# Optimization experiments

Measured on AMD Instinct MI355X. Metric: run time of the kernel, lower is better.

The kernel has to match this reference:

```python
import jax, jax.numpy as jnp
import numpy as np


def _normalize(x):
    # F.normalize(x, dim=-1): x / max(||x||_2, eps)
    n = jnp.linalg.norm(x, axis=-1, keepdims=True)
    return x / jnp.maximum(n, 1e-12)


def _clip_loss(i_sh, t_sh, scale, y):
    # Faithful, vectorized version of CLIP.forward (y: [B,1] int labels).
    i_n = _normalize(i_sh)
    t_n = _normalize(t_sh)
    logit_i2t = (i_n @ t_n.T) * scale            # [B,B]
    logit_t2i = t_n @ i_n.T                      # NOTE: no scale, as in source
    bs = i_sh.shape[0]
    yv = y.reshape(-1)                           # [B]
    # y.expand(bs,bs).T with y [bs,1] -> base[k,j] = y[j]
    base = jnp.broadcast_to(yv[None, :], (bs, bs)).astype(i_sh.dtype)
    flipped = jnp.where(base == 0, 1.0, 0.0)     # the inner loop flips 0<->nonzero
    label = jnp.where(yv[:, None] == 0, flipped, base)
    q = jax.nn.softmax(label / label.sum(axis=-1, keepdims=True), axis=-1)
    lq = jnp.log(q)
    lp1 = jax.nn.log_softmax(logit_i2t, axis=-1)
    lp2 = jax.nn.log_softmax(logit_t2i, axis=-1)
    # F.kl_div(input=log_pred, target, 'batchmean') = sum(target*(log(target)-input))/bs
    kl_p1_q = jnp.sum(q * (lq - lp1)) / bs
    kl_q_p1 = jnp.sum(jnp.exp(lp1) * (lp1 - lq)) / bs
    kl_p2_q = jnp.sum(q * (lq - lp2)) / bs
    kl_q_p2 = jnp.sum(jnp.exp(lp2) * (lp2 - lq)) / bs
    return (kl_p1_q + kl_q_p1 + kl_p2_q + kl_q_p2) / 4.0


def _forward(i, t, y, l1_w, l1_b, l2_w, l2_b, l3_w, l3_b, tl1_w, tl1_b, tl2_w, tl2_b,
             isp_w, isp_b, ish_w, ish_b, tsh_w, tsh_b, tsp_w, tsp_b,
             c1_w, c1_b, c2_w, c2_b, c3_w, c3_b, c4_w, c4_b, scale1, scale2):
    # ImgEncoder MLP head (penet backbone replaced by pooled 2048-d features;
    # dropout = identity, eval semantics)
    fi = jax.nn.relu(i @ l1_w.T + l1_b)
    fi = jax.nn.relu(fi @ l2_w.T + l2_b)
    fi = fi @ l3_w.T + l3_b                       # [B,128]
    # TabEncoder
    ft = jax.nn.relu(t @ tl1_w.T + tl1_b)
    ft = ft @ tl2_w.T + tl2_b                     # [B,128]
    loss1 = _clip_loss(fi, ft, jnp.exp(scale1), y)
    # SS heads
    i_sp = fi @ isp_w.T + isp_b
    i_sh = fi @ ish_w.T + ish_b
    t_sh = ft @ tsh_w.T + tsh_b
    t_sp = ft @ tsp_w.T + tsp_b
    # Separate: mean of Frobenius norms of BxB cross-Grams
    loss_sp = (jnp.linalg.norm(t_sp @ t_sh.T) + jnp.linalg.norm(i_sp @ i_sh.T)) / 2.0
    loss_sh = _clip_loss(i_sh, t_sh, jnp.exp(scale2), y)
    loss = (loss_sp + loss_sh + loss1) / 3.0
    i_sp_out = i_sp @ c1_w.T + c1_b
    i_sh_out = i_sh @ c2_w.T + c2_b
    t_sh_out = t_sh @ c3_w.T + c3_b
    t_sp_out = t_sp @ c4_w.T + c4_b
    return (loss, i_sp_out, i_sh_out, t_sp_out, t_sh_out)


def setup_inputs() -> dict:
    key = jax.random.key(0)
    ks = jax.random.split(key, 20)
    B = 4096

    def lin(k, out_d, in_d):  # kaiming-normal fan_out, relu
        return jax.random.normal(k, (out_d, in_d), jnp.float32) * np.sqrt(2.0 / out_d)

    log_scale = jnp.asarray(np.log(1.0 / 0.07), jnp.float32)
    return {
        'i': jax.random.normal(ks[0], (B, 2048), jnp.float32),
        't': jax.random.normal(ks[1], (B, 49), jnp.float32),
        'y': jax.random.randint(ks[2], (B, 1), 0, 2, jnp.int64 if jax.config.read('jax_enable_x64') else jnp.int32),
        'l1_w': lin(ks[3], 512, 2048), 'l1_b': jnp.zeros((512,), jnp.float32),
        'l2_w': lin(ks[4], 256, 512), 'l2_b': jnp.zeros((256,), jnp.float32),
        'l3_w': lin(ks[5], 128, 256), 'l3_b': jnp.zeros((128,), jnp.float32),
        'tl1_w': lin(ks[6], 128, 49), 'tl1_b': jnp.zeros((128,), jnp.float32),
        'tl2_w': lin(ks[7], 128, 128), 'tl2_b': jnp.zeros((128,), jnp.float32),
        'isp_w': lin(ks[8], 128, 128), 'isp_b': jnp.zeros((128,), jnp.float32),
        'ish_w': lin(ks[9], 128, 128), 'ish_b': jnp.zeros((128,), jnp.float32),
        'tsh_w': lin(ks[10], 128, 128), 'tsh_b': jnp.zeros((128,), jnp.float32),
        'tsp_w': lin(ks[11], 128, 128), 'tsp_b': jnp.zeros((128,), jnp.float32),
        'c1_w': lin(ks[12], 1, 128), 'c1_b': jnp.zeros((1,), jnp.float32),
        'c2_w': lin(ks[13], 1, 128), 'c2_b': jnp.zeros((1,), jnp.float32),
        'c3_w': lin(ks[14], 1, 128), 'c3_b': jnp.zeros((1,), jnp.float32),
        'c4_w': lin(ks[15], 1, 128), 'c4_b': jnp.zeros((1,), jnp.float32),
        'scale1': log_scale, 'scale2': log_scale,
    }


def reference(i, t, y, l1_w, l1_b, l2_w, l2_b, l3_w, l3_b, tl1_w, tl1_b, tl2_w, tl2_b,
              isp_w, isp_b, ish_w, ish_b, tsh_w, tsh_b, tsp_w, tsp_b,
              c1_w, c1_b, c2_w, c2_b, c3_w, c3_b, c4_w, c4_b, scale1, scale2):
    return _forward(i, t, y, l1_w, l1_b, l2_w, l2_b, l3_w, l3_b, tl1_w, tl1_b, tl2_w, tl2_b,
                    isp_w, isp_b, ish_w, ish_b, tsh_w, tsh_b, tsp_w, tsp_b,
                    c1_w, c1_b, c2_w, c2_b, c3_w, c3_b, c4_w, c4_b, scale1, scale2)
```

## Files before the change

### kernel.cpp

```cpp
#include <hip/hip_runtime.h>
#include <math.h>

#define BSZ 4096

typedef __attribute__((ext_vector_type(8))) short bf16x8;
typedef __attribute__((ext_vector_type(4))) float f32x4;

#define ST_ROW 0
#define ST_COL 786432
#define ST_T   1572864
#define ST_FLOATS 1589248

__device__ __forceinline__ unsigned short f2b(float f) {
    unsigned u = __float_as_uint(f);
    u = u + 0x7fffu + ((u >> 16) & 1u);
    return (unsigned short)(u >> 16);
}
__device__ __forceinline__ float b2f(unsigned short s) {
    return __uint_as_float(((unsigned)s) << 16);
}

__global__ void cast_all(const float* __restrict__ i_in,
                         const float* __restrict__ l1, const float* __restrict__ l2,
                         const float* __restrict__ l3, const float* __restrict__ tl2,
                         const float* __restrict__ isp, const float* __restrict__ ish,
                         const float* __restrict__ tsh, const float* __restrict__ tsp,
                         unsigned short* __restrict__ o) {
    int i = (blockIdx.x * 256 + threadIdx.x) * 4;
    if (i >= 9682944) return;
    const float* src; int off;
    if (i < 8388608)      { src = i_in; off = 0; }
    else if (i < 9437184) { src = l1;  off = 8388608; }
    else if (i < 9568256) { src = l2;  off = 9437184; }
    else if (i < 9601024) { src = l3;  off = 9568256; }
    else if (i < 9617408) { src = tl2; off = 9601024; }
    else if (i < 9633792) { src = isp; off = 9617408; }
    else if (i < 9650176) { src = ish; off = 9633792; }
    else if (i < 9666560) { src = tsh; off = 9650176; }
    else                  { src = tsp; off = 9666560; }
    float4 v = *(const float4*)(src + (i - off));
    ushort4 r;
    r.x = f2b(v.x); r.y = f2b(v.y); r.z = f2b(v.z); r.w = f2b(v.w);
    *(ushort4*)(o + i) = r;
}

__global__ void gemm_small(const float* __restrict__ A, const float* __restrict__ W,
                           const float* __restrict__ bias, unsigned short* __restrict__ C,
                           int M, int N, int K, int relu) {
    __shared__ float As[16][65];
    __shared__ float Ws[16][65];
    const int tx = threadIdx.x, ty = threadIdx.y;
    const int tid = ty * 16 + tx;
    const int m0 = blockIdx.y * 64, n0 = blockIdx.x * 64;
    float acc[4][4] = {};
    const int lrow = tid >> 2;
    const int lkb = (tid & 3) * 4;
    for (int k0 = 0; k0 < K; k0 += 16) {
#pragma unroll
        for (int u = 0; u < 4; ++u) {
            int k = k0 + lkb + u;
            As[lkb + u][lrow] = (k < K) ? A[(size_t)(m0 + lrow) * K + k] : 0.0f;
            Ws[lkb + u][lrow] = (k < K) ? W[(size_t)(n0 + lrow) * K + k] : 0.0f;
        }
        __syncthreads();
#pragma unroll
        for (int kk = 0; kk < 16; ++kk) {
            float av[4], bv[4];
#pragma unroll
            for (int i = 0; i < 4; ++i) av[i] = As[kk][ty * 4 + i];
#pragma unroll
            for (int j = 0; j < 4; ++j) bv[j] = Ws[kk][tx * 4 + j];
#pragma unroll
            for (int i = 0; i < 4; ++i)
#pragma unroll
                for (int j = 0; j < 4; ++j) acc[i][j] += av[i] * bv[j];
        }
        __syncthreads();
    }
#pragma unroll
    for (int i = 0; i < 4; ++i)
#pragma unroll
        for (int j = 0; j < 4; ++j) {
            int n = n0 + tx * 4 + j;
            float v = acc[i][j] + bias[n];
            if (relu) v = fmaxf(v, 0.0f);
            C[(size_t)(m0 + ty * 4 + i) * N + n] = f2b(v);
        }
}

__device__ __forceinline__ void mfma_loop(const unsigned short* __restrict__ A,
                                          const unsigned short* __restrict__ W,
                                          int K, int m0, int n0,
                                          short* As, short* Bs, f32x4 (&acc)[4][4]) {
    const int tid = threadIdx.x;
    const int w = tid >> 6, lane = tid & 63, quad = lane >> 4, l15 = lane & 15;
    const int rw = (w >> 1) * 64, cw = (w & 1) * 64;
    for (int k0 = 0; k0 < K; k0 += 64) {
#pragma unroll
        for (int r = 0; r < 4; ++r) {
            int idx = r * 256 + tid;
            int row = idx >> 3, cbp = idx & 7;
            int col = ((cbp ^ (row & 7)) << 3);
            *(bf16x8*)&As[row * 64 + cbp * 8] = *(const bf16x8*)&A[(size_t)(m0 + row) * K + k0 + col];
            *(bf16x8*)&Bs[row * 64 + cbp * 8] = *(const bf16x8*)&W[(size_t)(n0 + row) * K + k0 + col];
        }
        __syncthreads();
#pragma unroll
        for (int kb = 0; kb < 2; ++kb) {
            bf16x8 af[4], bfr[4];
            int cb = kb * 4 + quad;
#pragma unroll
            for (int i = 0; i < 4; ++i) {
                int row = rw + i * 16 + l15;
                af[i] = *(const bf16x8*)&As[row * 64 + ((cb ^ (row & 7)) << 3)];
            }
#pragma unroll
            for (int j = 0; j < 4; ++j) {
                int row = cw + j * 16 + l15;
                bfr[j] = *(const bf16x8*)&Bs[row * 64 + ((cb ^ (row & 7)) << 3)];
            }
#pragma unroll
            for (int i = 0; i < 4; ++i)
#pragma unroll
                for (int j = 0; j < 4; ++j)
                    acc[i][j] = __builtin_amdgcn_mfma_f32_16x16x32_bf16(af[i], bfr[j], acc[i][j], 0, 0, 0);
        }
        __syncthreads();
    }
}

__global__ __launch_bounds__(256) void mfma_gemm(const unsigned short* __restrict__ A,
                                                 const unsigned short* __restrict__ W,
                                                 const float* __restrict__ bias,
                                                 unsigned short* __restrict__ Cb,
                                                 int N, int K, int relu) {
    __shared__ alignas(16) short As[128 * 64];
    __shared__ alignas(16) short Bs[128 * 64];
    const int tid = threadIdx.x;
    const int w = tid >> 6, lane = tid & 63, quad = lane >> 4, l15 = lane & 15;
    const int rw = (w >> 1) * 64, cw = (w & 1) * 64;
    const int m0 = blockIdx.y * 128, n0 = blockIdx.x * 128;
    f32x4 acc[4][4];
#pragma unroll
    for (int i = 0; i < 4; ++i)
#pragma unroll
        for (int j = 0; j < 4; ++j) acc[i][j] = (f32x4){0.f, 0.f, 0.f, 0.f};
    mfma_loop(A, W, K, m0, n0, As, Bs, acc);
#pragma unroll
    for (int j = 0; j < 4; ++j) {
        int n = n0 + cw + j * 16 + l15;
        float bv = bias[n];
#pragma unroll
        for (int i = 0; i < 4; ++i)
#pragma unroll
            for (int r = 0; r < 4; ++r) {
                int m = m0 + rw + i * 16 + quad * 4 + r;
                float v = acc[i][j][r] + bv;
                if (relu) v = fmaxf(v, 0.f);
                Cb[(size_t)m * N + n] = f2b(v);
            }
    }
}

__global__ __launch_bounds__(256) void gemm34n(const unsigned short* __restrict__ FI2B,
                                               const unsigned short* __restrict__ FT1B,
                                               const unsigned short* __restrict__ WB,
                                               const float* __restrict__ l3_b,
                                               const float* __restrict__ tl2_b,
                                               unsigned short* __restrict__ FIB,
                                               unsigned short* __restrict__ FTB,
                                               unsigned short* __restrict__ FINB,
                                               unsigned short* __restrict__ FTNB) {
    __shared__ alignas(16) short As[128 * 64];
    __shared__ alignas(16) short Bs[128 * 64];
    __shared__ float rowss[128];
    const int tid = threadIdx.x;
    if (tid < 128) rowss[tid] = 0.f;
    const int z = blockIdx.z;
    const unsigned short* A = z ? FT1B : FI2B;
    const unsigned short* W = z ? (WB + 1212416) : (WB + 1179648);
    const float* bias = z ? tl2_b : l3_b;
    unsigned short* Cb = z ? FTB : FIB;
    unsigned short* CN = z ? FTNB : FINB;
    const int K = z ? 128 : 256;
    const int w = tid >> 6, lane = tid & 63, quad = lane >> 4, l15 = lane & 15;
    const int rw = (w >> 1) * 64, cw = (w & 1) * 64;
    const int m0 = blockIdx.y * 128;
    f32x4 acc[4][4];
#pragma unroll
    for (int i = 0; i < 4; ++i)
#pragma unroll
        for (int j = 0; j < 4; ++j) acc[i][j] = (f32x4){0.f, 0.f, 0.f, 0.f};
    mfma_loop(A, W, K, m0, 0, As, Bs, acc);
    float bv[4];
#pragma unroll
    for (int j = 0; j < 4; ++j) bv[j] = bias[cw + j * 16 + l15];
#pragma unroll
    for (int i = 0; i < 4; ++i)
#pragma unroll
        for (int r = 0; r < 4; ++r) {
            float ssp = 0.f;
#pragma unroll
            for (int j = 0; j < 4; ++j) {
                float v = acc[i][j][r] + bv[j];
                ssp += v * v;
            }
#pragma unroll
            for (int m = 1; m < 16; m <<= 1) ssp += __shfl_xor(ssp, m);
            if (l15 == 0) atomicAdd(&rowss[rw + i * 16 + quad * 4 + r], ssp);
        }
    __syncthreads();
#pragma unroll
    for (int i = 0; i < 4; ++i)
#pragma unroll
        for (int r = 0; r < 4; ++r) {
            int lrow = rw + i * 16 + quad * 4 + r;
            float inv = 1.f / fmaxf(sqrtf(rowss[lrow]), 1e-12f);
#pragma unroll
            for (int j = 0; j < 4; ++j) {
                int n = cw + j * 16 + l15;
                float v = acc[i][j][r] + bv[j];
                Cb[(size_t)(m0 + lrow) * 128 + n] = f2b(v);
                CN[(size_t)(m0 + lrow) * 128 + n] = f2b(v * inv);
            }
        }
}

__global__ __launch_bounds__(256) void heads4f(const unsigned short* __restrict__ FIB,
                                               const unsigned short* __restrict__ FTB,
                                               const unsigned short* __restrict__ WB,
                                               const float* __restrict__ bisp, const float* __restrict__ bish,
                                               const float* __restrict__ btsh, const float* __restrict__ btsp,
                                               const float* __restrict__ c1w, const float* __restrict__ c2w,
                                               const float* __restrict__ c3w, const float* __restrict__ c4w,
                                               const float* __restrict__ c1b, const float* __restrict__ c2b,
                                               const float* __restrict__ c3b, const float* __restrict__ c4b,
                                               float* __restrict__ ISP, float* __restrict__ ISH,
                                               float* __restrict__ TSH, float* __restrict__ TSP,
                                               unsigned short* __restrict__ ISHN,
                                               unsigned short* __restrict__ TSHN,
                                               float* __restrict__ out) {
    __shared__ alignas(16) short As[128 * 64];
    __shared__ alignas(16) short Bs[128 * 64];
    __shared__ float rowss[128];
    __shared__ float rowdot[128];
    const int tid = threadIdx.x;
    if (tid < 128) { rowss[tid] = 0.f; rowdot[tid] = 0.f; }
    const int z = blockIdx.z;
    const unsigned short* A = (z < 2) ? FIB : FTB;
    const unsigned short* W = WB + (z == 0 ? 1228800 : z == 1 ? 1245184 : z == 2 ? 1261568 : 1277952);
    const float* bias = z == 0 ? bisp : z == 1 ? bish : z == 2 ? btsh : btsp;
    const float* hw = z == 0 ? c1w : z == 1 ? c2w : z == 2 ? c3w : c4w;
    const float* hb = z == 0 ? c1b : z == 1 ? c2b : z == 2 ? c3b : c4b;
    float* Cf = z == 0 ? ISP : z == 1 ? ISH : z == 2 ? TSH : TSP;
    unsigned short* CN = z == 1 ? ISHN : z == 2 ? TSHN : nullptr;
    const int outoff = z == 0 ? 0 : z == 1 ? 1 : z == 2 ? 3 : 2;
    const int do_norm = (z == 1 || z == 2);
    const int w = tid >> 6, lane = tid & 63, quad = lane >> 4, l15 = lane & 15;
    const int rw = (w >> 1) * 64, cw = (w & 1) * 64;
    const int m0 = blockIdx.y * 128;
    f32x4 acc[4][4];
#pragma unroll
    for (int i = 0; i < 4; ++i)
#pragma unroll
        for (int j = 0; j < 4; ++j) acc[i][j] = (f32x4){0.f, 0.f, 0.f, 0.f};
    mfma_loop(A, W, 128, m0, 0, As, Bs, acc);
    float bv[4], wv[4];
#pragma unroll
    for (int j = 0; j < 4; ++j) {
        int n = cw + j * 16 + l15;
        bv[j] = bias[n];
        wv[j] = hw[n];
    }
#pragma unroll
    for (int i = 0; i < 4; ++i)
#pragma unroll
        for (int r = 0; r < 4; ++r) {
            float ssp = 0.f, dp = 0.f;
#pragma unroll
            for (int j = 0; j < 4; ++j) {
                float v = acc[i][j][r] + bv[j];
                ssp += v * v;
                dp += v * wv[j];
            }
#pragma unroll
            for (int m = 1; m < 16; m <<= 1) {
                ssp += __shfl_xor(ssp, m);
                dp += __shfl_xor(dp, m);
            }
            if (l15 == 0) {
                int lrow = rw + i * 16 + quad * 4 + r;
                atomicAdd(&rowdot[lrow], dp);
                if (do_norm) atomicAdd(&rowss[lrow], ssp);
            }
        }
    __syncthreads();
#pragma unroll
    for (int i = 0; i < 4; ++i)
#pragma unroll
        for (int r = 0; r < 4; ++r) {
            int lrow = rw + i * 16 + quad * 4 + r;
            float inv = do_norm ? (1.f / fmaxf(sqrtf(rowss[lrow]), 1e-12f)) : 0.f;
#pragma unroll
            for (int j = 0; j < 4; ++j) {
                int n = cw + j * 16 + l15;
                float v = acc[i][j][r] + bv[j];
                Cf[(size_t)(m0 + lrow) * 128 + n] = v;
                if (do_norm) CN[(size_t)(m0 + lrow) * 128 + n] = f2b(v * inv);
            }
        }
    if (tid < 128) out[1 + (size_t)outoff * BSZ + m0 + tid] = rowdot[tid] + hb[0];
}

__global__ __launch_bounds__(256) void clip_mfma(const unsigned short* __restrict__ In1,
                                                 const unsigned short* __restrict__ Tn1,
                                                 const unsigned short* __restrict__ In2,
                                                 const unsigned short* __restrict__ Tn2,
                                                 const int* __restrict__ y,
                                                 const float* __restrict__ scale_log1,
                                                 const float* __restrict__ scale_log2,
                                                 float* __restrict__ st1, float* __restrict__ st2) {
    __shared__ alignas(16) short As[128 * 64];
    __shared__ alignas(16) short Bs[128 * 64];
    const int z = blockIdx.z;
    const unsigned short* In = z ? In2 : In1;
    const unsigned short* Tn = z ? Tn2 : Tn1;
    const float* scale_log = z ? scale_log2 : scale_log1;
    float* st = z ? st2 : st1;
    const int tid = threadIdx.x;
    const int w = tid >> 6, lane = tid & 63, quad = lane >> 4, l15 = lane & 15;
    const int bx = blockIdx.x, by = blockIdx.y;
    const int r0 = by * 128, c0 = bx * 128;
    const int rw = (w >> 1) * 64, cw = (w & 1) * 64;
    f32x4 acc[4][4];
#pragma unroll
    for (int i = 0; i < 4; ++i)
#pragma unroll
        for (int j = 0; j < 4; ++j) acc[i][j] = (f32x4){0.f, 0.f, 0.f, 0.f};
    mfma_loop(In, Tn, 128, r0, c0, As, Bs, acc);

    const float s = expf(scale_log[0]);
    int yrow[4][4]; float mrow[4][4];
    int ycol[4];    float mcol[4];
#pragma unroll
    for (int i = 0; i < 4; ++i)
#pragma unroll
        for (int r = 0; r < 4; ++r) {
            int yy = y[r0 + rw + i * 16 + quad * 4 + r];
            yrow[i][r] = yy; mrow[i][r] = (yy == 0) ? 1.f : 0.f;
        }
#pragma unroll
    for (int j = 0; j < 4; ++j) {
        int yy = y[c0 + cw + j * 16 + l15];
        ycol[j] = yy; mcol[j] = (yy == 0) ? 1.f : 0.f;
    }
    float rZ[4][4] = {}, rF[4][4] = {}, rW[4][4] = {};
    float cZ[4] = {}, cE[4] = {}, cW[4] = {};
    float aAll = 0.f, aC0 = 0.f, aR0 = 0.f, aRC = 0.f;
#pragma unroll
    for (int i = 0; i < 4; ++i)
#pragma unroll
        for (int r = 0; r < 4; ++r) {
            float mr = mrow[i][r];
            int yr = yrow[i][r];
#pragma unroll
            for (int j = 0; j < 4; ++j) {
                float S = acc[i][j][r];
                float L = s * S;
                float e1 = __expf(L);
                float e2 = __expf(S);
                float msk = (yr == ycol[j]) ? 1.f : 0.f;
                rZ[i][r] += e1; rF[i][r] += e1 * L; rW[i][r] += e1 * msk;
                cZ[j] += e2;    cE[j] += e2 * S;    cW[j] += e2 * msk;
                float tmp = S * mcol[j];
                aAll += S; aC0 += tmp; aR0 += S * mr; aRC += tmp * mr;
            }
        }
    const int p_row = bx * 2 + (cw >> 6);
#pragma unroll
    for (int i = 0; i < 4; ++i)
#pragma unroll
        for (int r = 0; r < 4; ++r) {
#pragma unroll
            for (int m = 1; m < 16; m <<= 1) {
                rZ[i][r] += __shfl_xor(rZ[i][r], m);
                rF[i][r] += __shfl_xor(rF[i][r], m);
                rW[i][r] += __shfl_xor(rW[i][r], m);
            }
            if (l15 == (i * 4 + r)) {
                int grow = r0 + rw + i * 16 + quad * 4 + r;
                int base = ST_ROW + p_row * 4096 + grow;
                st[base]          = rZ[i][r];
                st[base + 262144] = rF[i][r];
                st[base + 524288] = rW[i][r];
            }
        }
    const int p_col = by * 2 + (rw >> 6);
#pragma unroll
    for (int j = 0; j < 4; ++j) {
        cZ[j] += __shfl_xor(cZ[j], 16); cZ[j] += __shfl_xor(cZ[j], 32);
        cE[j] += __shfl_xor(cE[j], 16); cE[j] += __shfl_xor(cE[j], 32);
        cW[j] += __shfl_xor(cW[j], 16); cW[j] += __shfl_xor(cW[j], 32);
        if (quad == 0) {
            int gcol = c0 + cw + j * 16 + l15;
            int base = ST_COL + p_col * 4096 + gcol;
            st[base]          = cZ[j];
            st[base + 262144] = cE[j];
            st[base + 524288] = cW[j];
        }
    }
#pragma unroll
    for (int m = 1; m < 64; m <<= 1) {
        aAll += __shfl_xor(aAll, m); aC0 += __shfl_xor(aC0, m);
        aR0 += __shfl_xor(aR0, m);   aRC += __shfl_xor(aRC, m);
    }
    if (lane == 0) {
        int wg = (by * 32 + bx) * 4 + w;
        float T00 = aRC, T01 = aR0 - aRC, T10 = aC0 - aRC, T11 = aAll - aR0 - aC0 + aRC;
        st[ST_T + wg * 4 + 0] = T00;
        st[ST_T + wg * 4 + 1] = T01;
        st[ST_T + wg * 4 + 2] = T10;
        st[ST_T + wg * 4 + 3] = T11;
    }
}

__global__ __launch_bounds__(256) void clip_finalize(const float* __restrict__ st1,
                                                     const float* __restrict__ st2,
                                                     const int* __restrict__ y,
                                                     float* __restrict__ RV,
                                                     float* __restrict__ TT) {
    __shared__ float cred[256];
    const int z = blockIdx.y;
    const float* st = z ? st2 : st1;
    const int tid = threadIdx.x;
    const int lane = tid & 63;
    const int k = blockIdx.x * 4 + (tid >> 6);
    const float Bf = (float)BSZ;

    float ccnt = 0.f;
    for (int i = tid; i < BSZ; i += 256) ccnt += (y[i] == 0) ? 1.f : 0.f;
    cred[tid] = ccnt;
    __syncthreads();
    for (int ss2 = 128; ss2 > 0; ss2 >>= 1) {
        if (tid < ss2) cred[tid] += cred[tid + ss2];
        __syncthreads();
    }
    const float n0 = cred[0];

    const int base = lane * 4096 + k;
    float Z1 = st[ST_ROW + base];
    float F1 = st[ST_ROW + 262144 + base];
    float W1 = st[ST_ROW + 524288 + base];
    float Z2 = st[ST_COL + base];
    float E2 = st[ST_COL + 262144 + base];
    float W2 = st[ST_COL + 524288 + base];
#pragma unroll
    for (int m = 1; m < 64; m <<= 1) {
        Z1 += __shfl_xor(Z1, m); F1 += __shfl_xor(F1, m); W1 += __shfl_xor(W1, m);
        Z2 += __shfl_xor(Z2, m); E2 += __shfl_xor(E2, m); W2 += __shfl_xor(W2, m);
    }
    if (lane == 0) {
        int yk = y[k];
        float n = (yk == 0) ? n0 : (Bf - n0);
        float a = 1.0f / n;
        float ea = expf(a);
        float denom = n * ea + (Bf - n);
        float q_s = ea / denom, q_d = 1.0f / denom;
        float ld = logf(denom);
        float lq_s = a - ld, lq_d = -ld;
        float Qlq = n * q_s * lq_s + (Bf - n) * q_d * lq_d;
        float term_r = Qlq + F1 / Z1 - lq_d - (lq_s - lq_d) * (W1 / Z1);
        float term_c = Qlq + E2 / Z2 - lq_d - (lq_s - lq_d) * (W2 / Z2);
        RV[(size_t)z * BSZ + k] = (term_r + term_c) / (4.0f * Bf);
    }
    if (blockIdx.x == 0) {
        __shared__ float4 tred[256];
        const float4* tp = (const float4*)&st[ST_T];
        float4 acc = {0.f, 0.f, 0.f, 0.f};
        for (int u = tid; u < 4096; u += 256) {
            float4 t4 = tp[u];
            acc.x += t4.x; acc.y += t4.y; acc.z += t4.z; acc.w += t4.w;
        }
        tred[tid] = acc;
        __syncthreads();
        for (int ss2 = 128; ss2 > 0; ss2 >>= 1) {
            if (tid < ss2) {
                tred[tid].x += tred[tid + ss2].x; tred[tid].y += tred[tid + ss2].y;
                tred[tid].z += tred[tid + ss2].z; tred[tid].w += tred[tid + ss2].w;
            }
            __syncthreads();
        }
        if (tid == 0) {
            TT[z * 4 + 0] = tred[0].x; TT[z * 4 + 1] = tred[0].y;
            TT[z * 4 + 2] = tred[0].z; TT[z * 4 + 3] = tred[0].w;
        }
    }
}

__global__ __launch_bounds__(256) void gram_splitk(const float* __restrict__ isp,
                                                   const float* __restrict__ ish,
                                                   const float* __restrict__ tsp,
                                                   const float* __restrict__ tsh,
                                                   float* __restrict__ GP) {
    __shared__ alignas(16) float As2[64][128];
    const int mat = blockIdx.y, chunk = blockIdx.x;
    const float* A = mat == 0 ? isp : mat == 1 ? ish : mat == 2 ? tsp : tsh;
    const int tid = threadIdx.x;
    const int m0 = chunk * 64;
#pragma unroll
    for (int r = 0; r < 8; ++r) {
        int idx = r * 256 + tid;
        int row = idx >> 5, c4 = (idx & 31) * 4;
        *(float4*)&As2[row][c4] = *(const float4*)&A[(size_t)(m0 + row) * 128 + c4];
    }
    __syncthreads();
    const int ty = tid >> 4, tx = tid & 15;
    float acc[8][8] = {};
    for (int k = 0; k < 64; ++k) {
        float av[8], bv[8];
        *(float4*)&av[0] = *(const float4*)&As2[k][ty * 8];
        *(float4*)&av[4] = *(const float4*)&As2[k][ty * 8 + 4];
        *(float4*)&bv[0] = *(const float4*)&As2[k][tx * 8];
        *(float4*)&bv[4] = *(const float4*)&As2[k][tx * 8 + 4];
#pragma unroll
        for (int i = 0; i < 8; ++i)
#pragma unroll
            for (int j = 0; j < 8; ++j) acc[i][j] += av[i] * bv[j];
    }
    float* Gp = GP + ((size_t)(mat * 64 + chunk) << 14);
#pragma unroll
    for (int i = 0; i < 8; ++i) {
        *(float4*)&Gp[(ty * 8 + i) * 128 + tx * 8]     = *(float4*)&acc[i][0];
        *(float4*)&Gp[(ty * 8 + i) * 128 + tx * 8 + 4] = *(float4*)&acc[i][4];
    }
}

__global__ void frob_combine(const float* __restrict__ GP, float* __restrict__ scal) {
    const int z = blockIdx.y;
    const int tid = threadIdx.x;
    int u = blockIdx.x * 256 + tid * 4;
    float4 ga = {0.f, 0.f, 0.f, 0.f};
    float4 gb = {0.f, 0.f, 0.f, 0.f};
    const size_t baseA = ((size_t)(2 * z) * 64) << 14;
    const size_t baseB = ((size_t)(2 * z + 1) * 64) << 14;
    for (int c = 0; c < 64; ++c) {
        float4 va = *(const float4*)&GP[baseA + ((size_t)c << 14) + u];
        float4 vb = *(const float4*)&GP[baseB + ((size_t)c << 14) + u];
        ga.x += va.x; ga.y += va.y; ga.z += va.z; ga.w += va.w;
        gb.x += vb.x; gb.y += vb.y; gb.z += vb.z; gb.w += vb.w;
    }
    float r = ga.x * gb.x + ga.y * gb.y + ga.z * gb.z + ga.w * gb.w;
#pragma unroll
    for (int m = 1; m < 64; m <<= 1) r += __shfl_xor(r, m);
    if (tid == 0) atomicAdd(&scal[3 + z], r);
}

__global__ void final_kernel(const float* __restrict__ RV, const float* __restrict__ scal,
                             const int* __restrict__ y,
                             const float* __restrict__ sl1, const float* __restrict__ sl2,
                             float* __restrict__ out) {
    __shared__ float red0[256], red1[256], red2[256];
    int tid = threadIdx.x;
    float s0 = 0.f, s1 = 0.f, cnt = 0.f;
    for (int u = tid; u < BSZ; u += 256) {
        s0 += RV[u]; s1 += RV[BSZ + u];
        cnt += (y[u] == 0) ? 1.f : 0.f;
    }
    red0[tid] = s0; red1[tid] = s1; red2[tid] = cnt;
    __syncthreads();
    for (int ss = 128; ss > 0; ss >>= 1) {
        if (tid < ss) {
            red0[tid] += red0[tid + ss]; red1[tid] += red1[tid + ss];
            red2[tid] += red2[tid + ss];
        }
        __syncthreads();
    }
    if (tid == 0) {
        const float Bf = (float)BSZ;
        float n0 = red2[0], n1 = Bf - n0;
        float e0 = expf(1.f / n0), e1 = expf(1.f / n1);
        float d0 = n0 * e0 + (Bf - n0), d1 = n1 * e1 + (Bf - n1);
        float qs0 = e0 / d0, qd0 = 1.f / d0, qs1 = e1 / d1, qd1 = 1.f / d1;
        float loss_z[2];
        for (int z = 0; z < 2; ++z) {
            float T00 = scal[8 + z * 4 + 0], T01 = scal[8 + z * 4 + 1];
            float T10 = scal[8 + z * 4 + 2], T11 = scal[8 + z * 4 + 3];
            float QS1 = qd0 * (T00 + T01) + (qs0 - qd0) * T00 + qd1 * (T10 + T11) + (qs1 - qd1) * T11;
            float QS2 = qd0 * (T00 + T10) + (qs0 - qd0) * T00 + qd1 * (T01 + T11) + (qs1 - qd1) * T11;
            float s = expf(z ? sl2[0] : sl1[0]);
            loss_z[z] = (z ? red1[0] : red0[0]) + (-s * QS1 - QS2) / (4.0f * Bf);
        }
        float loss_sp = 0.5f * (sqrtf(scal[4]) + sqrtf(scal[3]));
        out[0] = (loss_sp + loss_z[1] + loss_z[0]) / 3.0f;
    }
}

extern "C" void kernel_launch(void* const* d_in, const int* in_sizes, int n_in,
                              void* d_out, int out_size, void* d_ws, size_t ws_size,
                              hipStream_t stream) {
    const float* i_in  = (const float*)d_in[0];
    const float* t_in  = (const float*)d_in[1];
    const int*   y     = (const int*)d_in[2];
    const float* l1_w  = (const float*)d_in[3];
    const float* l1_b  = (const float*)d_in[4];
    const float* l2_w  = (const float*)d_in[5];
    const float* l2_b  = (const float*)d_in[6];
    const float* l3_w  = (const float*)d_in[7];
    const float* l3_b  = (const float*)d_in[8];
    const float* tl1_w = (const float*)d_in[9];
    const float* tl1_b = (const float*)d_in[10];
    const float* tl2_w = (const float*)d_in[11];
    const float* tl2_b = (const float*)d_in[12];
    const float* isp_w = (const float*)d_in[13];
    const float* isp_b = (const float*)d_in[14];
    const float* ish_w = (const float*)d_in[15];
    const float* ish_b = (const float*)d_in[16];
    const float* tsh_w = (const float*)d_in[17];
    const float* tsh_b = (const float*)d_in[18];
    const float* tsp_w = (const float*)d_in[19];
    const float* tsp_b = (const float*)d_in[20];
    const float* c1_w  = (const float*)d_in[21];
    const float* c1_b  = (const float*)d_in[22];
    const float* c2_w  = (const float*)d_in[23];
    const float* c2_b  = (const float*)d_in[24];
    const float* c3_w  = (const float*)d_in[25];
    const float* c3_b  = (const float*)d_in[26];
    const float* c4_w  = (const float*)d_in[27];
    const float* c4_b  = (const float*)d_in[28];
    const float* scale1 = (const float*)d_in[29];
    const float* scale2 = (const float*)d_in[30];

    float* ws = (float*)d_ws;
    float* SCAL = ws;
    float* RV   = ws + 64;
    float* ISP  = RV + 2 * BSZ;
    float* ISH  = ISP + (size_t)BSZ * 128;
    float* TSP  = ISH + (size_t)BSZ * 128;
    float* TSH  = TSP + (size_t)BSZ * 128;
    unsigned short* IB   = (unsigned short*)(TSH + (size_t)BSZ * 128);
    unsigned short* WB   = IB + (size_t)BSZ * 2048;
    unsigned short* FI1B = WB + 1294336;
    unsigned short* FI2B = FI1B + (size_t)BSZ * 512;
    unsigned short* FIB  = FI2B + (size_t)BSZ * 256;
    unsigned short* FT1B = FIB + (size_t)BSZ * 128;
    unsigned short* FTB  = FT1B + (size_t)BSZ * 128;
    unsigned short* FINB = FTB + (size_t)BSZ * 128;
    unsigned short* FTNB = FINB + (size_t)BSZ * 128;
    unsigned short* ISHN = FTNB + (size_t)BSZ * 128;
    unsigned short* TSHN = ISHN + (size_t)BSZ * 128;
    float* ST1 = (float*)IB;
    float* ST2 = ST1 + ST_FLOATS;
    float* GP = (float*)IB;

    float* out = (float*)d_out;

    hipMemsetAsync(d_ws, 0, 64 * sizeof(float), stream);
    cast_all<<<9456, 256, 0, stream>>>(i_in, l1_w, l2_w, l3_w, tl2_w, isp_w, ish_w, tsh_w, tsp_w, IB);
    gemm_small<<<dim3(2, 64), dim3(16, 16), 0, stream>>>(t_in, tl1_w, tl1_b, FT1B, BSZ, 128, 49, 1);

    mfma_gemm<<<dim3(4, 32), 256, 0, stream>>>(IB, WB, l1_b, FI1B, 512, 2048, 1);
    mfma_gemm<<<dim3(2, 32), 256, 0, stream>>>(FI1B, WB + 1048576, l2_b, FI2B, 256, 512, 1);
    gemm34n<<<dim3(1, 32, 2), 256, 0, stream>>>(FI2B, FT1B, WB, l3_b, tl2_b, FIB, FTB, FINB, FTNB);
    heads4f<<<dim3(1, 32, 4), 256, 0, stream>>>(FIB, FTB, WB, isp_b, ish_b, tsh_b, tsp_b,
                                                c1_w, c2_w, c3_w, c4_w, c1_b, c2_b, c3_b, c4_b,
                                                ISP, ISH, TSH, TSP, ISHN, TSHN, out);

    clip_mfma<<<dim3(32, 32, 2), 256, 0, stream>>>(FINB, FTNB, ISHN, TSHN, y, scale1, scale2, ST1, ST2);
    clip_finalize<<<dim3(1024, 2), 256, 0, stream>>>(ST1, ST2, y, RV, &SCAL[8]);

    gram_splitk<<<dim3(64, 4), 256, 0, stream>>>(ISP, ISH, TSP, TSH, GP);
    frob_combine<<<dim3(64, 2), 64, 0, stream>>>(GP, SCAL);
    final_kernel<<<1, 256, 0, stream>>>(RV, SCAL, y, scale1, scale2, out);
}
```

Baseline: 332.9 us.

## Merge small kernels, halve GEMM M-tile, and transpose clip stats layout

The cast and the small tabular GEMM now run in one launch, and the clip finalize and Gram split-K now share one launch, with GP moved to its own workspace region so the two do not overlap. The large MLP GEMMs switch to 64-row tiles, which doubles the grid for better CU occupancy at the cost of less reuse of the weight tile. The per-partition clip statistics are stored row-major (k*64+p), so the finalize reads them contiguously. Together this cuts launch overhead and idle tails, but the larger shared-memory footprint in post_kernel may reduce occupancy for the finalize blocks.

```diff
diff --git a/kernel.cpp b/kernel.cpp
--- a/kernel.cpp
+++ b/kernel.cpp
@@ -20,38 +20,40 @@
     return __uint_as_float(((unsigned)s) << 16);
 }
 
-__global__ void cast_all(const float* __restrict__ i_in,
-                         const float* __restrict__ l1, const float* __restrict__ l2,
-                         const float* __restrict__ l3, const float* __restrict__ tl2,
-                         const float* __restrict__ isp, const float* __restrict__ ish,
-                         const float* __restrict__ tsh, const float* __restrict__ tsp,
-                         unsigned short* __restrict__ o) {
-    int i = (blockIdx.x * 256 + threadIdx.x) * 4;
-    if (i >= 9682944) return;
-    const float* src; int off;
-    if (i < 8388608)      { src = i_in; off = 0; }
-    else if (i < 9437184) { src = l1;  off = 8388608; }
-    else if (i < 9568256) { src = l2;  off = 9437184; }
-    else if (i < 9601024) { src = l3;  off = 9568256; }
-    else if (i < 9617408) { src = tl2; off = 9601024; }
-    else if (i < 9633792) { src = isp; off = 9617408; }
-    else if (i < 9650176) { src = ish; off = 9633792; }
-    else if (i < 9666560) { src = tsh; off = 9650176; }
-    else                  { src = tsp; off = 9666560; }
-    float4 v = *(const float4*)(src + (i - off));
-    ushort4 r;
-    r.x = f2b(v.x); r.y = f2b(v.y); r.z = f2b(v.z); r.w = f2b(v.w);
-    *(ushort4*)(o + i) = r;
-}
-
-__global__ void gemm_small(const float* __restrict__ A, const float* __restrict__ W,
-                           const float* __restrict__ bias, unsigned short* __restrict__ C,
-                           int M, int N, int K, int relu) {
+__global__ void prep_kernel(const float* __restrict__ i_in,
+                            const float* __restrict__ l1, const float* __restrict__ l2,
+                            const float* __restrict__ l3, const float* __restrict__ tl2,
+                            const float* __restrict__ isp, const float* __restrict__ ish,
+                            const float* __restrict__ tsh, const float* __restrict__ tsp,
+                            unsigned short* __restrict__ o,
+                            const float* __restrict__ t_in, const float* __restrict__ tl1_w,
+                            const float* __restrict__ tl1_b, unsigned short* __restrict__ FT1B) {
     __shared__ float As[16][65];
     __shared__ float Ws[16][65];
-    const int tx = threadIdx.x, ty = threadIdx.y;
-    const int tid = ty * 16 + tx;
-    const int m0 = blockIdx.y * 64, n0 = blockIdx.x * 64;
+    if (blockIdx.x < 9456) {
+        int i = (blockIdx.x * 256 + threadIdx.x) * 4;
+        if (i >= 9682944) return;
+        const float* src; int off;
+        if (i < 8388608)      { src = i_in; off = 0; }
+        else if (i < 9437184) { src = l1;  off = 8388608; }
+        else if (i < 9568256) { src = l2;  off = 9437184; }
+        else if (i < 9601024) { src = l3;  off = 9568256; }
+        else if (i < 9617408) { src = tl2; off = 9601024; }
+        else if (i < 9633792) { src = isp; off = 9617408; }
+        else if (i < 9650176) { src = ish; off = 9633792; }
+        else if (i < 9666560) { src = tsh; off = 9650176; }
+        else                  { src = tsp; off = 9666560; }
+        float4 v = *(const float4*)(src + (i - off));
+        ushort4 r;
+        r.x = f2b(v.x); r.y = f2b(v.y); r.z = f2b(v.z); r.w = f2b(v.w);
+        *(ushort4*)(o + i) = r;
+        return;
+    }
+    const int b = blockIdx.x - 9456;
+    const int tid = threadIdx.x;
+    const int tx = tid & 15, ty = tid >> 4;
+    const int m0 = (b >> 1) * 64, n0 = (b & 1) * 64;
+    const int K = 49, N = 128;
     float acc[4][4] = {};
     const int lrow = tid >> 2;
     const int lkb = (tid & 3) * 4;
@@ -59,8 +61,8 @@
 #pragma unroll
         for (int u = 0; u < 4; ++u) {
             int k = k0 + lkb + u;
-            As[lkb + u][lrow] = (k < K) ? A[(size_t)(m0 + lrow) * K + k] : 0.0f;
-            Ws[lkb + u][lrow] = (k < K) ? W[(size_t)(n0 + lrow) * K + k] : 0.0f;
+            As[lkb + u][lrow] = (k < K) ? t_in[(size_t)(m0 + lrow) * K + k] : 0.0f;
+            Ws[lkb + u][lrow] = (k < K) ? tl1_w[(size_t)(n0 + lrow) * K + k] : 0.0f;
         }
         __syncthreads();
 #pragma unroll
@@ -82,9 +84,8 @@
 #pragma unroll
         for (int j = 0; j < 4; ++j) {
             int n = n0 + tx * 4 + j;
-            float v = acc[i][j] + bias[n];
-            if (relu) v = fmaxf(v, 0.0f);
-            C[(size_t)(m0 + ty * 4 + i) * N + n] = f2b(v);
+            float v = fmaxf(acc[i][j] + tl1_b[n], 0.0f);
+            FT1B[(size_t)(m0 + ty * 4 + i) * N + n] = f2b(v);
         }
 }
 
@@ -129,29 +130,66 @@
     }
 }
 
-__global__ __launch_bounds__(256) void mfma_gemm(const unsigned short* __restrict__ A,
-                                                 const unsigned short* __restrict__ W,
-                                                 const float* __restrict__ bias,
-                                                 unsigned short* __restrict__ Cb,
-                                                 int N, int K, int relu) {
-    __shared__ alignas(16) short As[128 * 64];
+__global__ __launch_bounds__(256) void mfma_gemm64(const unsigned short* __restrict__ A,
+                                                   const unsigned short* __restrict__ W,
+                                                   const float* __restrict__ bias,
+                                                   unsigned short* __restrict__ Cb,
+                                                   int N, int K, int relu) {
+    __shared__ alignas(16) short As[64 * 64];
     __shared__ alignas(16) short Bs[128 * 64];
     const int tid = threadIdx.x;
     const int w = tid >> 6, lane = tid & 63, quad = lane >> 4, l15 = lane & 15;
-    const int rw = (w >> 1) * 64, cw = (w & 1) * 64;
-    const int m0 = blockIdx.y * 128, n0 = blockIdx.x * 128;
-    f32x4 acc[4][4];
-#pragma unroll
-    for (int i = 0; i < 4; ++i)
+    const int rw = (w >> 1) * 32, cw = (w & 1) * 64;
+    const int m0 = blockIdx.y * 64, n0 = blockIdx.x * 128;
+    f32x4 acc[2][4];
+#pragma unroll
+    for (int i = 0; i < 2; ++i)
 #pragma unroll
         for (int j = 0; j < 4; ++j) acc[i][j] = (f32x4){0.f, 0.f, 0.f, 0.f};
-    mfma_loop(A, W, K, m0, n0, As, Bs, acc);
+    for (int k0 = 0; k0 < K; k0 += 64) {
+#pragma unroll
+        for (int r = 0; r < 2; ++r) {
+            int idx = r * 256 + tid;
+            int row = idx >> 3, cbp = idx & 7;
+            int col = ((cbp ^ (row & 7)) << 3);
+            *(bf16x8*)&As[row * 64 + cbp * 8] = *(const bf16x8*)&A[(size_t)(m0 + row) * K + k0 + col];
+        }
+#pragma unroll
+        for (int r = 0; r < 4; ++r) {
+            int idx = r * 256 + tid;
+            int row = idx >> 3, cbp = idx & 7;
+            int col = ((cbp ^ (row & 7)) << 3);
+            *(bf16x8*)&Bs[row * 64 + cbp * 8] = *(const bf16x8*)&W[(size_t)(n0 + row) * K + k0 + col];
+        }
+        __syncthreads();
+#pragma unroll
+        for (int kb = 0; kb < 2; ++kb) {
+            bf16x8 af[2], bfr[4];
+            int cb = kb * 4 + quad;
+#pragma unroll
+            for (int i = 0; i < 2; ++i) {
+                int row = rw + i * 16 + l15;
+                af[i] = *(const bf16x8*)&As[row * 64 + ((cb ^ (row & 7)) << 3)];
+            }
+#pragma unroll
+            for (int j = 0; j < 4; ++j) {
+                int row = cw + j * 16 + l15;
+                bfr[j] = *(const bf16x8*)&Bs[row * 64 + ((cb ^ (row & 7)) << 3)];
+            }
+#pragma unroll
+            for (int i = 0; i < 2; ++i)
+#pragma unroll
+                for (int j = 0; j < 4; ++j)
+                    acc[i][j] = __builtin_amdgcn_mfma_f32_16x16x32_bf16(af[i], bfr[j], acc[i][j], 0, 0, 0);
+        }
+        __syncthreads();
+    }
 #pragma unroll
     for (int j = 0; j < 4; ++j) {
         int n = n0 + cw + j * 16 + l15;
         float bv = bias[n];
 #pragma unroll
-        for (int i = 0; i < 4; ++i)
+        for (int i = 0; i < 2; ++i)
 #pragma unroll
             for (int r = 0; r < 4; ++r) {
                 int m = m0 + rw + i * 16 + quad * 4 + r;
@@ -389,7 +427,7 @@
             }
             if (l15 == (i * 4 + r)) {
                 int grow = r0 + rw + i * 16 + quad * 4 + r;
-                int base = ST_ROW + p_row * 4096 + grow;
+                int base = ST_ROW + grow * 64 + p_row;
                 st[base]          = rZ[i][r];
                 st[base + 262144] = rF[i][r];
                 st[base + 524288] = rW[i][r];
@@ -403,7 +441,7 @@
         cW[j] += __shfl_xor(cW[j], 16); cW[j] += __shfl_xor(cW[j], 32);
         if (quad == 0) {
             int gcol = c0 + cw + j * 16 + l15;
-            int base = ST_COL + p_col * 4096 + gcol;
+            int base = ST_COL + gcol * 64 + p_col;
             st[base]          = cZ[j];
             st[base + 262144] = cE[j];
             st[base + 524288] = cW[j];
@@ -424,15 +462,56 @@
     }
 }
 
-__global__ __launch_bounds__(256) void clip_finalize(const float* __restrict__ st1,
-                                                     const float* __restrict__ st2,
-                                                     const int* __restrict__ y,
-                                                     float* __restrict__ RV,
-                                                     float* __restrict__ TT) {
-    __shared__ float cred[256];
+__global__ __launch_bounds__(256) void post_kernel(const float* __restrict__ st1,
+                                                   const float* __restrict__ st2,
+                                                   const int* __restrict__ y,
+                                                   float* __restrict__ RV,
+                                                   float* __restrict__ TT,
+                                                   const float* __restrict__ isp,
+                                                   const float* __restrict__ ish,
+                                                   const float* __restrict__ tsp,
+                                                   const float* __restrict__ tsh,
+                                                   float* __restrict__ GP) {
+    __shared__ alignas(16) float sh[64 * 128];
+    const int tid = threadIdx.x;
+    if (blockIdx.y == 2) {
+        if (blockIdx.x >= 256) return;
+        float (*As2)[128] = (float(*)[128])sh;
+        const int mat = blockIdx.x >> 6, chunk = blockIdx.x & 63;
+        const float* A = mat == 0 ? isp : mat == 1 ? ish : mat == 2 ? tsp : tsh;
+        const int m0 = chunk * 64;
+#pragma unroll
+        for (int r = 0; r < 8; ++r) {
+            int idx = r * 256 + tid;
+            int row = idx >> 5, c4 = (idx & 31) * 4;
+            *(float4*)&As2[row][c4] = *(const float4*)&A[(size_t)(m0 + row) * 128 + c4];
+        }
+        __syncthreads();
+        const int ty = tid >> 4, tx = tid & 15;
+        float acc[8][8] = {};
+        for (int k = 0; k < 64; ++k) {
+            float av[8], bv[8];
+            *(float4*)&av[0] = *(const float4*)&As2[k][ty * 8];
+            *(float4*)&av[4] = *(const float4*)&As2[k][ty * 8 + 4];
+            *(float4*)&bv[0] = *(const float4*)&As2[k][tx * 8];
+            *(float4*)&bv[4] = *(const float4*)&As2[k][tx * 8 + 4];
+#pragma unroll
+            for (int i = 0; i < 8; ++i)
+#pragma unroll
+                for (int j = 0; j < 8; ++j) acc[i][j] += av[i] * bv[j];
+        }
+        float* Gp = GP + ((size_t)(mat * 64 + chunk) << 14);
+#pragma unroll
+        for (int i = 0; i < 8; ++i) {
+            *(float4*)&Gp[(ty * 8 + i) * 128 + tx * 8]     = *(float4*)&acc[i][0];
+            *(float4*)&Gp[(ty * 8 + i) * 128 + tx * 8 + 4] = *(float4*)&acc[i][4];
+        }
+        return;
+    }
+    float* cred = sh;
+    float4* tred = (float4*)(sh + 256);
     const int z = blockIdx.y;
     const float* st = z ? st2 : st1;
-    const int tid = threadIdx.x;
     const int lane = tid & 63;
     const int k = blockIdx.x * 4 + (tid >> 6);
     const float Bf = (float)BSZ;
@@ -447,7 +526,7 @@
     }
     const float n0 = cred[0];
 
-    const int base = lane * 4096 + k;
+    const int base = k * 64 + lane;
     float Z1 = st[ST_ROW + base];
     float F1 = st[ST_ROW + 262144 + base];
     float W1 = st[ST_ROW + 524288 + base];
@@ -474,7 +553,6 @@
         RV[(size_t)z * BSZ + k] = (term_r + term_c) / (4.0f * Bf);
     }
     if (blockIdx.x == 0) {
-        __shared__ float4 tred[256];
         const float4* tp = (const float4*)&st[ST_T];
         float4 acc = {0.f, 0.f, 0.f, 0.f};
         for (int u = tid; u < 4096; u += 256) {
@@ -494,44 +572,6 @@
             TT[z * 4 + 0] = tred[0].x; TT[z * 4 + 1] = tred[0].y;
             TT[z * 4 + 2] = tred[0].z; TT[z * 4 + 3] = tred[0].w;
         }
-    }
-}
-
-__global__ __launch_bounds__(256) void gram_splitk(const float* __restrict__ isp,
-                                                   const float* __restrict__ ish,
-                                                   const float* __restrict__ tsp,
-                                                   const float* __restrict__ tsh,
-                                                   float* __restrict__ GP) {
-    __shared__ alignas(16) float As2[64][128];
-    const int mat = blockIdx.y, chunk = blockIdx.x;
-    const float* A = mat == 0 ? isp : mat == 1 ? ish : mat == 2 ? tsp : tsh;
-    const int tid = threadIdx.x;
-    const int m0 = chunk * 64;
-#pragma unroll
-    for (int r = 0; r < 8; ++r) {
-        int idx = r * 256 + tid;
-        int row = idx >> 5, c4 = (idx & 31) * 4;
-        *(float4*)&As2[row][c4] = *(const float4*)&A[(size_t)(m0 + row) * 128 + c4];
-    }
-    __syncthreads();
-    const int ty = tid >> 4, tx = tid & 15;
-    float acc[8][8] = {};
-    for (int k = 0; k < 64; ++k) {
-        float av[8], bv[8];
-        *(float4*)&av[0] = *(const float4*)&As2[k][ty * 8];
-        *(float4*)&av[4] = *(const float4*)&As2[k][ty * 8 + 4];
-        *(float4*)&bv[0] = *(const float4*)&As2[k][tx * 8];
-        *(float4*)&bv[4] = *(const float4*)&As2[k][tx * 8 + 4];
-#pragma unroll
-        for (int i = 0; i < 8; ++i)
-#pragma unroll
-            for (int j = 0; j < 8; ++j) acc[i][j] += av[i] * bv[j];
-    }
-    float* Gp = GP + ((size_t)(mat * 64 + chunk) << 14);
-#pragma unroll
-    for (int i = 0; i < 8; ++i) {
-        *(float4*)&Gp[(ty * 8 + i) * 128 + tx * 8]     = *(float4*)&acc[i][0];
-        *(float4*)&Gp[(ty * 8 + i) * 128 + tx * 8 + 4] = *(float4*)&acc[i][4];
     }
 }
 
@@ -650,25 +690,21 @@
     unsigned short* TSHN = ISHN + (size_t)BSZ * 128;
     float* ST1 = (float*)IB;
     float* ST2 = ST1 + ST_FLOATS;
-    float* GP = (float*)IB;
+    float* GP  = ST2 + ST_FLOATS;
 
     float* out = (float*)d_out;
 
     hipMemsetAsync(d_ws, 0, 64 * sizeof(float), stream);
-    cast_all<<<9456, 256, 0, stream>>>(i_in, l1_w, l2_w, l3_w, tl2_w, isp_w, ish_w, tsh_w, tsp_w, IB);
-    gemm_small<<<dim3(2, 64), dim3(16, 16), 0, stream>>>(t_in, tl1_w, tl1_b, FT1B, BSZ, 128, 49, 1);
-
-    mfma_gemm<<<dim3(4, 32), 256, 0, stream>>>(IB, WB, l1_b, FI1B, 512, 2048, 1);
-    mfma_gemm<<<dim3(2, 32), 256, 0, stream>>>(FI1B, WB + 1048576, l2_b, FI2B, 256, 512, 1);
+    prep_kernel<<<9584, 256, 0, stream>>>(i_in, l1_w, l2_w, l3_w, tl2_w, isp_w, ish_w, tsh_w, tsp_w,
+                                          IB, t_in, tl1_w, tl1_b, FT1B);
+    mfma_gemm64<<<dim3(4, 64), 256, 0, stream>>>(IB, WB, l1_b, FI1B, 512, 2048, 1);
+    mfma_gemm64<<<dim3(2, 64), 256, 0, stream>>>(FI1B, WB + 1048576, l2_b, FI2B, 256, 512, 1);
     gemm34n<<<dim3(1, 32, 2), 256, 0, stream>>>(FI2B, FT1B, WB, l3_b, tl2_b, FIB, FTB, FINB, FTNB);
     heads4f<<<dim3(1, 32, 4), 256, 0, stream>>>(FIB, FTB, WB, isp_b, ish_b, tsh_b, tsp_b,
                                                 c1_w, c2_w, c3_w, c4_w, c1_b, c2_b, c3_b, c4_b,
                                                 ISP, ISH, TSH, TSP, ISHN, TSHN, out);
-
     clip_mfma<<<dim3(32, 32, 2), 256, 0, stream>>>(FINB, FTNB, ISHN, TSHN, y, scale1, scale2, ST1, ST2);
-    clip_finalize<<<dim3(1024, 2), 256, 0, stream>>>(ST1, ST2, y, RV, &SCAL[8]);
-
-    gram_splitk<<<dim3(64, 4), 256, 0, stream>>>(ISP, ISH, TSP, TSH, GP);
+    post_kernel<<<dim3(1024, 3), 256, 0, stream>>>(ST1, ST2, y, RV, &SCAL[8], ISP, ISH, TSP, TSH, GP);
     frob_combine<<<dim3(64, 2), 64, 0, stream>>>(GP, SCAL);
     final_kernel<<<1, 256, 0, stream>>>(RV, SCAL, y, scale1, scale2, out);
 }
```

Measured after the change: 306.9 us. 1.08x faster.
